# Optimization experiments

Measured on AMD Instinct MI355X. Metric: run time of the kernel, lower is better.

The kernel has to match this reference:

```python
import jax, jax.numpy as jnp
import numpy as np

NUM_HEADS = 8
OUT_DIM = 128
DEPTH = OUT_DIM // NUM_HEADS  # 16


def setup_inputs() -> dict:
    key = jax.random.key(0)
    ks = jax.random.split(key, 6)
    B, N, F_IN = 32, 512, 64
    x = jax.random.normal(ks[0], (B, N, F_IN), dtype=jnp.float32)
    adj = jax.random.uniform(ks[1], (B, N, N), dtype=jnp.float32)
    wq = jax.random.normal(ks[2], (F_IN, OUT_DIM), dtype=jnp.float32) * 0.05
    wk = jax.random.normal(ks[3], (F_IN, OUT_DIM), dtype=jnp.float32) * 0.05
    wv = jax.random.normal(ks[4], (F_IN, OUT_DIM), dtype=jnp.float32) * 0.05
    wo = jax.random.normal(ks[5], (OUT_DIM, OUT_DIM), dtype=jnp.float32) * 0.05
    return {"x": x, "adj": adj, "wq": wq, "wk": wk, "wv": wv, "wo": wo}


def _split_heads(t, B, N):
    # [B, N, out_dim] -> [B, H, N, D]
    return t.reshape(B, N, NUM_HEADS, DEPTH).transpose(0, 2, 1, 3)


def reference(x, adj, wq, wk, wv, wo):
    B, N, _ = x.shape
    q = _split_heads(x @ wq, B, N)  # [B,H,N,D]
    k = _split_heads(x @ wk, B, N)
    v = _split_heads(x @ wv, B, N)
    scale = jnp.sqrt(jnp.float32(DEPTH))
    scores = jnp.einsum("bhnd,bhmd->bhnm", q, k) / scale  # [B,H,N,N]
    attn = jnp.tanh(scores * adj[:, None, :, :])  # mask-multiply + tanh
    h = jnp.einsum("bhnm,bhmd->bhnd", attn, v)  # [B,H,N,D]
    h = h.transpose(0, 2, 1, 3).reshape(B, N, OUT_DIM)
    return jax.nn.relu(h @ wo)
```

## Files before the change

kernel.cpp:

```cpp
#include <hip/hip_runtime.h>


typedef __bf16 bf16x8 __attribute__((ext_vector_type(8)));
typedef __bf16 bf16x4 __attribute__((ext_vector_type(4)));
typedef float  f32x4  __attribute__((ext_vector_type(4)));

#define MFMA16(a, b, c) __builtin_amdgcn_mfma_f32_16x16x32_bf16((a), (b), (c), 0, 0, 0)

__global__ __launch_bounds__(256) void prep_kernel(
    const float* __restrict__ wq, const float* __restrict__ wk,
    const float* __restrict__ wv, const float* __restrict__ wo,
    __bf16* __restrict__ WTb, __bf16* __restrict__ WoTb)
{
    int idx = blockIdx.x * 256 + threadIdx.x;
    if (idx < 6144) {
        int j4 = idx % 96, k = idx / 96, j = j4 * 4;
        const float* w = (j < 128) ? wq : ((j < 256) ? wk : wv);
        f32x4 v = *(const f32x4*)&w[k * 128 + (j & 127)];
#pragma unroll
        for (int e = 0; e < 4; ++e) WTb[(j + e) * 64 + k] = (__bf16)v[e];
    } else if (idx < 6144 + 4096) {
        int i2 = idx - 6144;
        int j4 = i2 % 32, k = i2 / 32, j = j4 * 4;
        f32x4 v = *(const f32x4*)&wo[k * 128 + j];
#pragma unroll
        for (int e = 0; e < 4; ++e) WoTb[(j + e) * 128 + k] = (__bf16)v[e];
    }
}

__global__ __launch_bounds__(256) void qkv_kernel(
    const float* __restrict__ x, const __bf16* __restrict__ WTb,
    __bf16* __restrict__ Qb, __bf16* __restrict__ Kb, __bf16* __restrict__ VT)
{
    const int tid = threadIdx.x, lane = tid & 63, w = tid >> 6;
    const int g = lane >> 4, lr = lane & 15;
    const long R0 = (long)blockIdx.x * 16;
    const int b = (int)(R0 >> 9);
    const int nloc = (int)(R0 & 511) + g * 4;

    bf16x8 af[2];
#pragma unroll
    for (int kk = 0; kk < 2; ++kk) {
        const float* xp = x + (R0 + lr) * 64 + kk * 32 + g * 8;
        f32x4 x0 = *(const f32x4*)xp, x1 = *(const f32x4*)(xp + 4);
        bf16x8 a;
#pragma unroll
        for (int e = 0; e < 4; ++e) { a[e] = (__bf16)x0[e]; a[4 + e] = (__bf16)x1[e]; }
        af[kk] = a;
    }

#pragma unroll 2
    for (int i = 0; i < 6; ++i) {
        const int j0 = (w * 6 + i) * 16;
        f32x4 acc = {0.f, 0.f, 0.f, 0.f};
#pragma unroll
        for (int kk = 0; kk < 2; ++kk) {
            bf16x8 bf = *(const bf16x8*)&WTb[(j0 + lr) * 64 + kk * 32 + g * 8];
            acc = MFMA16(af[kk], bf, acc);
        }
        const int jj = (j0 + lr) & 127, hh = jj >> 4, d = jj & 15;
        const int bh = b * 8 + hh, t = j0 >> 7;
        if (t == 2) {
            bf16x4 pk;
#pragma unroll
            for (int r = 0; r < 4; ++r) pk[r] = (__bf16)acc[r];
            *(bf16x4*)&VT[((long)bh * 16 + d) * 512 + nloc] = pk;
        } else {
            __bf16* dst = t ? Kb : Qb;
#pragma unroll
            for (int r = 0; r < 4; ++r)
                dst[((long)bh * 512 + nloc + r) * 16 + d] = (__bf16)acc[r];
        }
    }
}

__device__ __forceinline__ float tanh_q(float sadj) {
    const float C = 0.7213475204444817f;
    float e = __builtin_amdgcn_exp2f(sadj * C);
    return 1.0f - 2.0f * __builtin_amdgcn_rcpf(e + 1.0f);
}

__global__ __launch_bounds__(512) void attn_kernel(
    const float* __restrict__ adj,
    const __bf16* __restrict__ Qb, const __bf16* __restrict__ Kb,
    const __bf16* __restrict__ VT, __bf16* __restrict__ Hb)
{
    __shared__ __align__(16) float adjL[16][512];

    const int tid  = threadIdx.x;
    const int lane = tid & 63;
    const int h    = tid >> 6;
    const int g    = lane >> 4;
    const int lr   = lane & 15;
    const int b    = blockIdx.y;
    const int n0   = blockIdx.x * 16;
    const int bh   = b * 8 + h;

    const char* strip = (const char*)(adj + ((long)b * 512 + n0) * 512);
    f32x4 tmp[4];
#pragma unroll
    for (int i = 0; i < 4; ++i)
        tmp[i] = *(const f32x4*)(strip + i * 8192 + tid * 16);
#pragma unroll
    for (int i = 0; i < 4; ++i) {
        int o = i * 8192 + tid * 16;
        int row = o >> 11, col = o & 2047;
        *(f32x4*)((char*)adjL + row * 2048 + (col ^ ((row & 7) << 4))) = tmp[i];
    }

    bf16x8 qf = {};
    if (g < 2) qf = *(const bf16x8*)&Qb[((long)bh * 512 + n0 + lr) * 16 + g * 8];

    const __bf16* Kbase = Kb + (long)bh * 512 * 16;
    const __bf16* Vrow  = VT + ((long)bh * 16 + lr) * 512;
    const char*   aRow  = (const char*)adjL + lr * 2048;
    const int     sw    = (lr & 7) << 4;

    __syncthreads();

    f32x4 accH = {0.f, 0.f, 0.f, 0.f};
#pragma unroll 2
    for (int t = 0; t < 16; ++t) {
        const int m0 = t * 32;
        bf16x8 kf0 = {}, kf1 = {};
        if (g < 2) {
            kf0 = *(const bf16x8*)&Kbase[(m0 + lr) * 16 + g * 8];
            kf1 = *(const bf16x8*)&Kbase[(m0 + 16 + lr) * 16 + g * 8];
        }
        bf16x4 v0 = *(const bf16x4*)&Vrow[m0 + g * 4];
        bf16x4 v1 = *(const bf16x4*)&Vrow[m0 + 16 + g * 4];
        f32x4 a0 = *(const f32x4*)(aRow + (((m0 + g * 4) * 4) ^ sw));
        f32x4 a1 = *(const f32x4*)(aRow + (((m0 + 16 + g * 4) * 4) ^ sw));

        const f32x4 z = {0.f, 0.f, 0.f, 0.f};
        f32x4 s0 = MFMA16(kf0, qf, z);
        f32x4 s1 = MFMA16(kf1, qf, z);

        bf16x8 paf, vf;
#pragma unroll
        for (int r = 0; r < 4; ++r) {
            paf[r]     = (__bf16)tanh_q(s0[r] * a0[r]);
            paf[4 + r] = (__bf16)tanh_q(s1[r] * a1[r]);
            vf[r]      = v0[r];
            vf[4 + r]  = v1[r];
        }
        accH = MFMA16(paf, vf, accH);
    }

#pragma unroll
    for (int r = 0; r < 4; ++r)
        Hb[((long)b * 512 + n0 + g * 4 + r) * 128 + h * 16 + lr] = (__bf16)accH[r];
}

__global__ __launch_bounds__(256) void oproj_kernel(
    const __bf16* __restrict__ Hb, const __bf16* __restrict__ WoTb,
    float* __restrict__ out)
{
    const int tid = threadIdx.x, lane = tid & 63, w = tid >> 6;
    const int g = lane >> 4, lr = lane & 15;
    const long R0 = (long)blockIdx.x * 16;

    bf16x8 af[4];
#pragma unroll
    for (int kk = 0; kk < 4; ++kk)
        af[kk] = *(const bf16x8*)&Hb[(R0 + lr) * 128 + kk * 32 + g * 8];

#pragma unroll
    for (int i = 0; i < 2; ++i) {
        const int j0 = w * 32 + i * 16;
        f32x4 acc = {0.f, 0.f, 0.f, 0.f};
#pragma unroll
        for (int kk = 0; kk < 4; ++kk) {
            bf16x8 bf = *(const bf16x8*)&WoTb[(j0 + lr) * 128 + kk * 32 + g * 8];
            acc = MFMA16(af[kk], bf, acc);
        }
#pragma unroll
        for (int r = 0; r < 4; ++r)
            out[(R0 + g * 4 + r) * 128 + j0 + lr] = fmaxf(acc[r], 0.f);
    }
}

extern "C" void kernel_launch(void* const* d_in, const int* in_sizes, int n_in,
                              void* d_out, int out_size, void* d_ws, size_t ws_size,
                              hipStream_t stream) {
    const float* x   = (const float*)d_in[0];
    const float* adj = (const float*)d_in[1];
    const float* wq  = (const float*)d_in[2];
    const float* wk  = (const float*)d_in[3];
    const float* wv  = (const float*)d_in[4];
    const float* wo  = (const float*)d_in[5];
    float* out = (float*)d_out;

    char* wsb = (char*)d_ws;
    __bf16* WTb  = (__bf16*)wsb;
    __bf16* WoTb = (__bf16*)(wsb + 49152);
    __bf16* Qb   = (__bf16*)(wsb + 81920);
    __bf16* Kb   = Qb + 2097152;
    __bf16* VT   = Kb + 2097152;
    __bf16* Hb   = VT + 2097152;

    prep_kernel<<<40, 256, 0, stream>>>(wq, wk, wv, wo, WTb, WoTb);
    qkv_kernel<<<1024, 256, 0, stream>>>(x, WTb, Qb, Kb, VT);
    attn_kernel<<<dim3(32, 32), 512, 0, stream>>>(adj, Qb, Kb, VT, Hb);
    oproj_kernel<<<1024, 256, 0, stream>>>(Hb, WoTb, out);
}
```

Before: 143.1 us.

## Process 32 query rows per attention block with software-pipelined K/V/adj tile loads

Each attention block now handles 32 query rows instead of 16, so every K and V fragment loaded from global memory feeds two score and accumulate MFMA chains. The inner loop is restructured into a double-buffered load/compute pipeline that issues the next tile's loads before computing the current one. This halves the grid to 512 blocks and doubles the LDS adj strip to 64KB per block, which lowers the number of resident blocks and raises register pressure. The launch-bounds hint also requests a minimum of 4 waves per SIMD.

```diff
diff --git a/kernel.cpp b/kernel.cpp
--- a/kernel.cpp
+++ b/kernel.cpp
@@ -80,12 +80,61 @@
     return 1.0f - 2.0f * __builtin_amdgcn_rcpf(e + 1.0f);
 }
 
-__global__ __launch_bounds__(512) void attn_kernel(
+struct Tile {
+    bf16x8 kf0, kf1;
+    bf16x4 v0, v1;
+    f32x4 a00, a01, a10, a11;
+};
+
+__device__ __forceinline__ Tile load_tile(
+    int m0, bool gactive, const __bf16* Kbase, int lr, int g,
+    const __bf16* Vrow, const char* aRow0, const char* aRow1, int sw)
+{
+    Tile t;
+    t.kf0 = {}; t.kf1 = {};
+    if (gactive) {
+        t.kf0 = *(const bf16x8*)&Kbase[(m0 + lr) * 16 + g * 8];
+        t.kf1 = *(const bf16x8*)&Kbase[(m0 + 16 + lr) * 16 + g * 8];
+    }
+    t.v0 = *(const bf16x4*)&Vrow[m0 + g * 4];
+    t.v1 = *(const bf16x4*)&Vrow[m0 + 16 + g * 4];
+    const int c0 = ((m0 + g * 4) * 4) ^ sw;
+    const int c1 = ((m0 + 16 + g * 4) * 4) ^ sw;
+    t.a00 = *(const f32x4*)(aRow0 + c0);
+    t.a01 = *(const f32x4*)(aRow0 + c1);
+    t.a10 = *(const f32x4*)(aRow1 + c0);
+    t.a11 = *(const f32x4*)(aRow1 + c1);
+    return t;
+}
+
+__device__ __forceinline__ void compute_tile(
+    const Tile& t, bf16x8 qf0, bf16x8 qf1, f32x4& acc0, f32x4& acc1)
+{
+    const f32x4 z = {0.f, 0.f, 0.f, 0.f};
+    f32x4 s00 = MFMA16(t.kf0, qf0, z);
+    f32x4 s01 = MFMA16(t.kf1, qf0, z);
+    f32x4 s10 = MFMA16(t.kf0, qf1, z);
+    f32x4 s11 = MFMA16(t.kf1, qf1, z);
+    bf16x8 p0, p1, vf;
+#pragma unroll
+    for (int r = 0; r < 4; ++r) {
+        p0[r]     = (__bf16)tanh_q(s00[r] * t.a00[r]);
+        p0[4 + r] = (__bf16)tanh_q(s01[r] * t.a01[r]);
+        p1[r]     = (__bf16)tanh_q(s10[r] * t.a10[r]);
+        p1[4 + r] = (__bf16)tanh_q(s11[r] * t.a11[r]);
+        vf[r]     = t.v0[r];
+        vf[4 + r] = t.v1[r];
+    }
+    acc0 = MFMA16(p0, vf, acc0);
+    acc1 = MFMA16(p1, vf, acc1);
+}
+
+__global__ __launch_bounds__(512, 4) void attn_kernel(
     const float* __restrict__ adj,
     const __bf16* __restrict__ Qb, const __bf16* __restrict__ Kb,
     const __bf16* __restrict__ VT, __bf16* __restrict__ Hb)
 {
-    __shared__ __align__(16) float adjL[16][512];
+    __shared__ __align__(16) float adjL[32][512];
 
     const int tid  = threadIdx.x;
     const int lane = tid & 63;
@@ -93,63 +142,53 @@
     const int g    = lane >> 4;
     const int lr   = lane & 15;
     const int b    = blockIdx.y;
-    const int n0   = blockIdx.x * 16;
+    const int n0   = blockIdx.x * 32;
     const int bh   = b * 8 + h;
 
     const char* strip = (const char*)(adj + ((long)b * 512 + n0) * 512);
-    f32x4 tmp[4];
-#pragma unroll
-    for (int i = 0; i < 4; ++i)
+    f32x4 tmp[8];
+#pragma unroll
+    for (int i = 0; i < 8; ++i)
         tmp[i] = *(const f32x4*)(strip + i * 8192 + tid * 16);
 #pragma unroll
-    for (int i = 0; i < 4; ++i) {
+    for (int i = 0; i < 8; ++i) {
         int o = i * 8192 + tid * 16;
         int row = o >> 11, col = o & 2047;
         *(f32x4*)((char*)adjL + row * 2048 + (col ^ ((row & 7) << 4))) = tmp[i];
     }
 
-    bf16x8 qf = {};
-    if (g < 2) qf = *(const bf16x8*)&Qb[((long)bh * 512 + n0 + lr) * 16 + g * 8];
+    const bool ga = (g < 2);
+    bf16x8 qf0 = {}, qf1 = {};
+    if (ga) {
+        qf0 = *(const bf16x8*)&Qb[((long)bh * 512 + n0 + lr) * 16 + g * 8];
+        qf1 = *(const bf16x8*)&Qb[((long)bh * 512 + n0 + 16 + lr) * 16 + g * 8];
+    }
 
     const __bf16* Kbase = Kb + (long)bh * 512 * 16;
     const __bf16* Vrow  = VT + ((long)bh * 16 + lr) * 512;
-    const char*   aRow  = (const char*)adjL + lr * 2048;
+    const char*   aRow0 = (const char*)adjL + lr * 2048;
+    const char*   aRow1 = (const char*)adjL + (16 + lr) * 2048;
     const int     sw    = (lr & 7) << 4;
 
     __syncthreads();
 
-    f32x4 accH = {0.f, 0.f, 0.f, 0.f};
-#pragma unroll 2
-    for (int t = 0; t < 16; ++t) {
-        const int m0 = t * 32;
-        bf16x8 kf0 = {}, kf1 = {};
-        if (g < 2) {
-            kf0 = *(const bf16x8*)&Kbase[(m0 + lr) * 16 + g * 8];
-            kf1 = *(const bf16x8*)&Kbase[(m0 + 16 + lr) * 16 + g * 8];
-        }
-        bf16x4 v0 = *(const bf16x4*)&Vrow[m0 + g * 4];
-        bf16x4 v1 = *(const bf16x4*)&Vrow[m0 + 16 + g * 4];
-        f32x4 a0 = *(const f32x4*)(aRow + (((m0 + g * 4) * 4) ^ sw));
-        f32x4 a1 = *(const f32x4*)(aRow + (((m0 + 16 + g * 4) * 4) ^ sw));
-
-        const f32x4 z = {0.f, 0.f, 0.f, 0.f};
-        f32x4 s0 = MFMA16(kf0, qf, z);
-        f32x4 s1 = MFMA16(kf1, qf, z);
-
-        bf16x8 paf, vf;
-#pragma unroll
-        for (int r = 0; r < 4; ++r) {
-            paf[r]     = (__bf16)tanh_q(s0[r] * a0[r]);
-            paf[4 + r] = (__bf16)tanh_q(s1[r] * a1[r]);
-            vf[r]      = v0[r];
-            vf[4 + r]  = v1[r];
-        }
-        accH = MFMA16(paf, vf, accH);
-    }
-
-#pragma unroll
-    for (int r = 0; r < 4; ++r)
-        Hb[((long)b * 512 + n0 + g * 4 + r) * 128 + h * 16 + lr] = (__bf16)accH[r];
+    f32x4 acc0 = {0.f, 0.f, 0.f, 0.f}, acc1 = {0.f, 0.f, 0.f, 0.f};
+
+    Tile tA = load_tile(0, ga, Kbase, lr, g, Vrow, aRow0, aRow1, sw);
+#pragma unroll 1
+    for (int t = 0; t < 16; t += 2) {
+        Tile tB = load_tile((t + 1) * 32, ga, Kbase, lr, g, Vrow, aRow0, aRow1, sw);
+        compute_tile(tA, qf0, qf1, acc0, acc1);
+        if (t + 2 < 16)
+            tA = load_tile((t + 2) * 32, ga, Kbase, lr, g, Vrow, aRow0, aRow1, sw);
+        compute_tile(tB, qf0, qf1, acc0, acc1);
+    }
+
+#pragma unroll
+    for (int r = 0; r < 4; ++r) {
+        Hb[((long)b * 512 + n0 + g * 4 + r) * 128 + h * 16 + lr]      = (__bf16)acc0[r];
+        Hb[((long)b * 512 + n0 + 16 + g * 4 + r) * 128 + h * 16 + lr] = (__bf16)acc1[r];
+    }
 }
 
 __global__ __launch_bounds__(256) void oproj_kernel(
@@ -201,6 +240,6 @@
 
     prep_kernel<<<40, 256, 0, stream>>>(wq, wk, wv, wo, WTb, WoTb);
     qkv_kernel<<<1024, 256, 0, stream>>>(x, WTb, Qb, Kb, VT);
-    attn_kernel<<<dim3(32, 32), 512, 0, stream>>>(adj, Qb, Kb, VT, Hb);
+    attn_kernel<<<dim3(16, 32), 512, 0, stream>>>(adj, Qb, Kb, VT, Hb);
     oproj_kernel<<<1024, 256, 0, stream>>>(Hb, WoTb, out);
 }
```

New measurement: 128.5 us. 10.2% less time.
